# Kernel tuning notes

Measured on AMD Instinct MI355X. Metric: run time of the kernel, lower is better.

## Reference

```python
import jax, jax.numpy as jnp
import numpy as np

DIM = 1024
HEADS = 16
DH = DIM // HEADS          # 64
SEQ_LEN = 4096
LATENT = 1024
HIST = SEQ_LEN - LATENT    # 3072
LN_EPS = 1e-5


def setup_inputs() -> dict:
    key = jax.random.key(0)
    ks = jax.random.split(key, 5)
    b = 2
    x = jax.random.normal(ks[0], (b, SEQ_LEN, DIM), dtype=jnp.float32)
    s = 0.02
    Wq = jax.random.normal(ks[1], (DIM, DIM), dtype=jnp.float32) * s
    Wkv = jax.random.normal(ks[2], (DIM, DIM), dtype=jnp.float32) * s
    Wo = jax.random.normal(ks[3], (DIM, DIM), dtype=jnp.float32) * s
    bo = jnp.zeros((DIM,), dtype=jnp.float32)
    gamma = jnp.ones((DH,), dtype=jnp.float32)
    beta = jnp.zeros((DH,), dtype=jnp.float32)
    return {"x": x, "Wq": Wq, "Wkv": Wkv, "Wo": Wo, "bo": bo,
            "gamma": gamma, "beta": beta}


def _rotate_half(t):
    t1, t2 = jnp.split(t, 2, axis=-1)
    return jnp.concatenate([-t2, t1], axis=-1)


def reference(x, Wq, Wkv, Wo, bo, gamma, beta):
    b, n, dim = x.shape
    # projections (nn.Linear: y = x @ W.T), split heads -> (b, h, n, d)
    q = jnp.einsum('bnd,ed->bne', x, Wq).reshape(b, n, HEADS, DH).transpose(0, 2, 1, 3)
    kv = jnp.einsum('bnd,ed->bne', x, Wkv).reshape(b, n, HEADS, DH).transpose(0, 2, 1, 3)

    # layer_num == 0: queries only for the latent segment
    q = q[:, :, HIST:, :]  # (b, h, latent, d)

    # rotary embeddings: concat-style freqs over head dim
    inv_freq = 1.0 / (10000.0 ** (jnp.arange(0, DH, 2, dtype=jnp.float32) / DH))
    freqs = jnp.arange(n, dtype=jnp.float32)[:, None] * inv_freq[None, :]  # (n, DH/2)
    emb = jnp.concatenate([freqs, freqs], axis=-1)  # (n, DH)
    cos, sin = jnp.cos(emb), jnp.sin(emb)
    q = q * cos[HIST:] + _rotate_half(q) * sin[HIST:]
    kv = kv * cos + _rotate_half(kv) * sin

    q = q * (DH ** -0.5)

    # per-kv LayerNorm over head dim
    mu = kv.mean(axis=-1, keepdims=True)
    var = ((kv - mu) ** 2).mean(axis=-1, keepdims=True)
    kvn = (kv - mu) * jax.lax.rsqrt(var + LN_EPS) * gamma + beta

    attn = jnp.einsum('bhid,bhjd->bhij', q, kvn)  # (b, h, latent, n)

    # causal mask only on latent columns: col j (>= HIST) masked if j-HIST > i
    i = jnp.arange(LATENT)[:, None]
    j = jnp.arange(n)[None, :]
    mask = (j - HIST) > i  # false for history columns (j < HIST)
    neg = -jnp.finfo(attn.dtype).max
    attn = jnp.where(mask, neg, attn)

    attn = jax.nn.softmax(attn, axis=-1)
    out = jnp.einsum('bhij,bhjd->bhid', attn, kvn)  # (b, h, latent, d)
    out = out.transpose(0, 2, 1, 3).reshape(b, LATENT, dim)
    return jnp.einsum('bnd,ed->bne', out, Wo) + bo
```

## Files before the change

kernel.cpp:

```cpp
#include <hip/hip_runtime.h>
#include <hip/hip_bf16.h>
#include <cstdint>

#define DIMC 1024
#define HEADS 16
#define DHH 64
#define SEQ 4096
#define LATENT 1024
#define HISTC 3072
#define BATCH 2

typedef __attribute__((ext_vector_type(8))) __bf16 bf16x8;
typedef __attribute__((ext_vector_type(4))) float f32x4;
typedef __attribute__((ext_vector_type(16))) float f32x16;

__global__ void k_prep(const float* __restrict__ x, const float* __restrict__ Wq,
                       const float* __restrict__ Wkv, const float* __restrict__ Wo,
                       __bf16* __restrict__ x16, __bf16* __restrict__ wq16,
                       __bf16* __restrict__ wkv16, __bf16* __restrict__ wo16,
                       float2* __restrict__ cs) {
  int bidx = blockIdx.x;
  if (bidx < 2048) {
    int base = bidx * 256 + threadIdx.x;
#pragma unroll
    for (int k = 0; k < 4; ++k) {
      int i = base + k * 524288;
      float4 v = reinterpret_cast<const float4*>(x)[i];
      union { __bf16 h[4]; uint64_t u; } p;
      p.h[0] = (__bf16)v.x; p.h[1] = (__bf16)v.y;
      p.h[2] = (__bf16)v.z; p.h[3] = (__bf16)v.w;
      reinterpret_cast<uint64_t*>(x16)[i] = p.u;
    }
  } else if (bidx < 3584) {
    int id = bidx - 2048;
    const float* src; __bf16* dst;
    if (id < 512) { src = Wq; dst = wq16; }
    else if (id < 1024) { src = Wkv; dst = wkv16; id -= 512; }
    else { src = Wo; dst = wo16; id -= 1024; }
#pragma unroll
    for (int k = 0; k < 2; ++k) {
      int idx = id * 512 + k * 256 + threadIdx.x;
      float4 v = reinterpret_cast<const float4*>(src)[idx];
      union { __bf16 h[4]; uint64_t u; } p;
      p.h[0] = (__bf16)v.x; p.h[1] = (__bf16)v.y;
      p.h[2] = (__bf16)v.z; p.h[3] = (__bf16)v.w;
      reinterpret_cast<uint64_t*>(dst)[idx] = p.u;
    }
  } else {
    int idx = (bidx - 3584) * 256 + threadIdx.x;
    int pos = idx >> 5, f = idx & 31;
    float invf = exp2f(-(float)f * 0.41524101186f);
    float s, c;
    sincosf((float)pos * invf, &s, &c);
    cs[idx] = make_float2(c, s);
  }
}

__device__ __forceinline__ void gload16(void* lds, const void* g) {
  __builtin_amdgcn_global_load_lds(
      (const __attribute__((address_space(1))) unsigned int*)g,
      (__attribute__((address_space(3))) unsigned int*)lds, 16, 0, 0);
}

template<int BIAS>
__launch_bounds__(256)
__global__ void k_gemm(const __bf16* __restrict__ A, const __bf16* __restrict__ Bw,
                       float* __restrict__ C, const float* __restrict__ bias,
                       int M, int N, int K) {
  __shared__ __align__(16) char lds[32768];
  const int t = threadIdx.x;
  const int l = t & 63, w = t >> 6;
  const int wr = w >> 1, wc = w & 1;
  const int mblocks = M >> 7;
  const int m0 = (blockIdx.x % mblocks) * 128, n0 = (blockIdx.x / mblocks) * 128;
  const int lrow = l & 15, lk = l >> 4;
  f32x4 acc[4][4] = {};

  for (int k0 = 0; k0 < K; k0 += 64) {
    if (k0) __syncthreads();
#pragma unroll
    for (int i = 0; i < 4; ++i) {
      int c = i * 256 + t;
      int row = c >> 3;
      int kgc = ((c & 7) ^ (row & 7)) * 8;
      gload16(lds + c * 16, A + (size_t)(m0 + row) * K + k0 + kgc);
      gload16(lds + 16384 + c * 16, Bw + (size_t)(n0 + row) * K + k0 + kgc);
    }
    __syncthreads();
#pragma unroll
    for (int ks = 0; ks < 2; ++ks) {
      bf16x8 af[4], bfr[4];
#pragma unroll
      for (int m = 0; m < 4; ++m) {
        int row = wr * 64 + m * 16 + lrow;
        af[m] = *reinterpret_cast<const bf16x8*>(
            lds + row * 128 + ((ks * 4 + lk) ^ (row & 7)) * 16);
      }
#pragma unroll
      for (int n = 0; n < 4; ++n) {
        int row = wc * 64 + n * 16 + lrow;
        bfr[n] = *reinterpret_cast<const bf16x8*>(
            lds + 16384 + row * 128 + ((ks * 4 + lk) ^ (row & 7)) * 16);
      }
#pragma unroll
      for (int m = 0; m < 4; ++m)
#pragma unroll
        for (int n = 0; n < 4; ++n)
          acc[m][n] = __builtin_amdgcn_mfma_f32_16x16x32_bf16(af[m], bfr[n], acc[m][n], 0, 0, 0);
    }
  }

#pragma unroll
  for (int m = 0; m < 4; ++m)
#pragma unroll
    for (int n = 0; n < 4; ++n)
#pragma unroll
      for (int r = 0; r < 4; ++r) {
        int row = m0 + wr * 64 + m * 16 + (l >> 4) * 4 + r;
        int col = n0 + wc * 64 + n * 16 + (l & 15);
        float v = acc[m][n][r];
        if (BIAS) v += bias[col];
        C[(size_t)row * N + col] = v;
      }
}

__launch_bounds__(256)
__global__ void k_gemmqkv(const __bf16* __restrict__ x16,
                          const __bf16* __restrict__ wkv16,
                          const __bf16* __restrict__ wq16,
                          __bf16* __restrict__ kvn, __bf16* __restrict__ kvnT,
                          __bf16* __restrict__ qb,
                          const float* __restrict__ gamma,
                          const float* __restrict__ beta,
                          const float2* __restrict__ cstab) {
  __shared__ __align__(16) char lds[32768];
  const int t = threadIdx.x, l = t & 63, w = t >> 6;
  const int wr = w >> 1, wc = w & 1;
  const int by = blockIdx.x % 80;
  const bool isq = by >= 64;
  const int m0 = (isq ? (by - 64) : by) * 128;
  const int n0 = (blockIdx.x / 80) * 128;
  const __bf16* Bw = isq ? wq16 : wkv16;
  const int lrow = l & 15, lk = l >> 4;
  f32x4 acc[4][4] = {};

  for (int k0 = 0; k0 < 1024; k0 += 64) {
    if (k0) __syncthreads();
#pragma unroll
    for (int i = 0; i < 4; ++i) {
      int c = i * 256 + t;
      int row = c >> 3;
      int kgc = ((c & 7) ^ (row & 7)) * 8;
      int mi = m0 + row;
      if (isq) mi += HISTC + (mi >> 10) * HISTC;
      gload16(lds + c * 16, x16 + (size_t)mi * 1024 + k0 + kgc);
      gload16(lds + 16384 + c * 16, Bw + (size_t)(n0 + row) * 1024 + k0 + kgc);
    }
    __syncthreads();
#pragma unroll
    for (int ks = 0; ks < 2; ++ks) {
      bf16x8 af[4], bfr[4];
#pragma unroll
      for (int m = 0; m < 4; ++m) {
        int row = wr * 64 + m * 16 + lrow;
        af[m] = *reinterpret_cast<const bf16x8*>(
            lds + row * 128 + ((ks * 4 + lk) ^ (row & 7)) * 16);
      }
#pragma unroll
      for (int n = 0; n < 4; ++n) {
        int row = wc * 64 + n * 16 + lrow;
        bfr[n] = *reinterpret_cast<const bf16x8*>(
            lds + 16384 + row * 128 + ((ks * 4 + lk) ^ (row & 7)) * 16);
      }
#pragma unroll
      for (int m = 0; m < 4; ++m)
#pragma unroll
        for (int n = 0; n < 4; ++n)
          acc[m][n] = __builtin_amdgcn_mfma_f32_16x16x32_bf16(af[m], bfr[n], acc[m][n], 0, 0, 0);
    }
  }

#pragma unroll
  for (int m = 0; m < 4; ++m)
#pragma unroll
    for (int r = 0; r < 4; ++r) {
      int rl = wr * 64 + m * 16 + lk * 4 + r;
      int pos = isq ? (HISTC + ((m0 + rl) & 1023)) : ((m0 + rl) & 4095);
      float2 cs0 = cstab[pos * 32 + lrow];
      float2 cs1 = cstab[pos * 32 + 16 + lrow];
      float a0 = acc[m][0][r], a2 = acc[m][2][r];
      acc[m][0][r] = a0 * cs0.x - a2 * cs0.y;
      acc[m][2][r] = a2 * cs0.x + a0 * cs0.y;
      float a1 = acc[m][1][r], a3 = acc[m][3][r];
      acc[m][1][r] = a1 * cs1.x - a3 * cs1.y;
      acc[m][3][r] = a3 * cs1.x + a1 * cs1.y;
    }

  const int h = (n0 + wc * 64) >> 6;
  if (!isq) {
    float g4[4], b4[4];
#pragma unroll
    for (int n = 0; n < 4; ++n) { g4[n] = gamma[n * 16 + lrow]; b4[n] = beta[n * 16 + lrow]; }
#pragma unroll
    for (int m = 0; m < 4; ++m)
#pragma unroll
      for (int r = 0; r < 4; ++r) {
        float s1 = acc[m][0][r] + acc[m][1][r] + acc[m][2][r] + acc[m][3][r];
        float s2 = acc[m][0][r] * acc[m][0][r] + acc[m][1][r] * acc[m][1][r] +
                   acc[m][2][r] * acc[m][2][r] + acc[m][3][r] * acc[m][3][r];
#pragma unroll
        for (int mk = 1; mk < 16; mk <<= 1) {
          s1 += __shfl_xor(s1, mk);
          s2 += __shfl_xor(s2, mk);
        }
        float mu = s1 * 0.015625f;
        float var = s2 * 0.015625f - mu * mu;
        float inv = rsqrtf(var + 1e-5f);
#pragma unroll
        for (int n = 0; n < 4; ++n)
          acc[m][n][r] = (acc[m][n][r] - mu) * inv * g4[n] + b4[n];
      }
    const size_t hb = (size_t)((m0 >> 12) * HEADS + h);
#pragma unroll
    for (int m = 0; m < 4; ++m)
#pragma unroll
      for (int r = 0; r < 4; ++r) {
        int pos = (m0 + wr * 64 + m * 16 + lk * 4 + r) & 4095;
#pragma unroll
        for (int n = 0; n < 4; ++n)
          kvn[(hb * SEQ + pos) * DHH + n * 16 + lrow] = (__bf16)acc[m][n][r];
      }
#pragma unroll
    for (int m = 0; m < 4; ++m) {
      int pos0 = (m0 + wr * 64 + m * 16 + lk * 4) & 4095;
      int sp = (pos0 & ~12) | ((pos0 & 4) << 1) | ((pos0 & 8) >> 1);
#pragma unroll
      for (int n = 0; n < 4; ++n) {
        union { __bf16 hh[4]; uint64_t u; } pk;
#pragma unroll
        for (int r = 0; r < 4; ++r) pk.hh[r] = (__bf16)acc[m][n][r];
        *reinterpret_cast<uint64_t*>(kvnT + (hb * DHH + n * 16 + lrow) * SEQ + sp) = pk.u;
      }
    }
  } else {
    const size_t hb = (size_t)((m0 >> 10) * HEADS + h);
#pragma unroll
    for (int m = 0; m < 4; ++m)
#pragma unroll
      for (int r = 0; r < 4; ++r) {
        int qi = (m0 + wr * 64 + m * 16 + lk * 4 + r) & 1023;
#pragma unroll
        for (int n = 0; n < 4; ++n)
          qb[(hb * LATENT + qi) * DHH + n * 16 + lrow] =
              (__bf16)(acc[m][n][r] * 0.18033688011112042f);
      }
  }
}

__device__ __forceinline__ float fexp2(float x) {
#if __has_builtin(__builtin_amdgcn_exp2f)
  return __builtin_amdgcn_exp2f(x);
#else
  return exp2f(x);
#endif
}

__device__ __forceinline__ unsigned pk2(float a, float b) {
  union { __bf16 h[2]; unsigned u; } x;
  x.h[0] = (__bf16)a; x.h[1] = (__bf16)b;
  return x.u;
}

template<int NJ>
__launch_bounds__(256)
__global__ void k_flash12(const __bf16* __restrict__ qb, const __bf16* __restrict__ kvn,
                          const __bf16* __restrict__ kvnT, float* __restrict__ part) {
  const int bid = blockIdx.x;
  const int xcd = bid & 7;
  const int u = bid >> 3;
  const int jq = u % NJ;
  const int rest = u / NJ;
  int itq = rest & 7;
  const int grpb = rest >> 3;
  if (grpb >= 2) itq = 7 - itq;
  const int bh = xcd + 8 * grpb;
  const int h = bh & 15, b = bh >> 4;
  const int t = threadIdx.x, l = t & 63, w = t >> 6;
  const int q = l & 31, hi = l >> 5;
  const int iw0 = itq * 128;
  const int iwv = iw0 + w * 32;
  const int i = iwv + q;
  const __bf16* qbase = qb + ((size_t)(b * HEADS + h) * LATENT + iwv) * DHH;
  const __bf16* kbase = kvn + (size_t)(b * HEADS + h) * SEQ * DHH;
  const __bf16* vbase = kvnT + (size_t)(b * HEADS + h) * DHH * SEQ;

  __shared__ __align__(16) __bf16 Kl[2][2][32][64];
  __shared__ __align__(16) __bf16 Vl[2][2][64][32];

  const int krow = t >> 3, kgc = ((t & 7) ^ (krow & 7)) * 8;
  const int vrow = t >> 2, vgc = ((t & 3) ^ (vrow & 3)) * 8;

  bf16x8 qf[4];
#pragma unroll
  for (int c = 0; c < 4; ++c)
    qf[c] = *reinterpret_cast<const bf16x8*>(qbase + (size_t)q * DHH + c * 16 + hi * 8);

  const f32x16 Z = {};
  f32x16 O0 = {}, O1 = {};
  float m_run = -INFINITY, lacc = 0.f;

  const int ng = 2 * itq + 50;
  const int g0 = (ng * jq) / NJ, g1 = (ng * (jq + 1)) / NJ;
  const int sx = q & 3;

  {
    const int ja = g0 * 64;
    gload16((char*)&Kl[0][0][0][0] + t * 16, kbase + (size_t)(ja + krow) * DHH + kgc);
    gload16((char*)&Kl[0][1][0][0] + t * 16, kbase + (size_t)(ja + 32 + krow) * DHH + kgc);
    gload16((char*)&Vl[0][0][0][0] + t * 16, vbase + (size_t)vrow * SEQ + ja + vgc);
    gload16((char*)&Vl[0][1][0][0] + t * 16, vbase + (size_t)vrow * SEQ + ja + 32 + vgc);
  }
  __syncthreads();

  for (int g = g0; g < g1; ++g) {
    const int cur = (g - g0) & 1;
    const int ja = g * 64, jb = ja + 32;
    const char* Ka = (const char*)&Kl[cur][0][0][0];
    const char* Va = (const char*)&Vl[cur][0][0][0];
    bf16x8 kf0 = *reinterpret_cast<const bf16x8*>(Ka + q * 128 + ((0 + hi) ^ (q & 7)) * 16);
    bf16x8 kf1 = *reinterpret_cast<const bf16x8*>(Ka + q * 128 + ((2 + hi) ^ (q & 7)) * 16);
    bf16x8 kf2 = *reinterpret_cast<const bf16x8*>(Ka + q * 128 + ((4 + hi) ^ (q & 7)) * 16);
    bf16x8 kf3 = *reinterpret_cast<const bf16x8*>(Ka + q * 128 + ((6 + hi) ^ (q & 7)) * 16);
    f32x16 S = __builtin_amdgcn_mfma_f32_32x32x16_bf16(kf0, qf[0], Z, 0, 0, 0);
    S = __builtin_amdgcn_mfma_f32_32x32x16_bf16(kf1, qf[1], S, 0, 0, 0);
    S = __builtin_amdgcn_mfma_f32_32x32x16_bf16(kf2, qf[2], S, 0, 0, 0);
    S = __builtin_amdgcn_mfma_f32_32x32x16_bf16(kf3, qf[3], S, 0, 0, 0);
    if (g + 1 < g1) {
      const int jn = (g + 1) * 64;
      gload16((char*)&Kl[cur ^ 1][0][0][0] + t * 16, kbase + (size_t)(jn + krow) * DHH + kgc);
      gload16((char*)&Kl[cur ^ 1][1][0][0] + t * 16, kbase + (size_t)(jn + 32 + krow) * DHH + kgc);
      gload16((char*)&Vl[cur ^ 1][0][0][0] + t * 16, vbase + (size_t)vrow * SEQ + jn + vgc);
      gload16((char*)&Vl[cur ^ 1][1][0][0] + t * 16, vbase + (size_t)vrow * SEQ + jn + 32 + vgc);
    }
    if (ja + 31 > iwv + HISTC) {
#pragma unroll
      for (int r = 0; r < 16; ++r) {
        int j = ja + (r & 3) + 8 * (r >> 2) + 4 * hi;
        if (j > i + HISTC) S[r] = -1e30f;
      }
    }
    {
      float u1 = fmaxf(fmaxf(S[0], S[1]), S[2]);
      float u2 = fmaxf(fmaxf(S[3], S[4]), S[5]);
      float u3 = fmaxf(fmaxf(S[6], S[7]), S[8]);
      float u4 = fmaxf(fmaxf(S[9], S[10]), S[11]);
      float u5 = fmaxf(fmaxf(S[12], S[13]), S[14]);
      float pm = fmaxf(fmaxf(fmaxf(u1, u2), u3), fmaxf(fmaxf(u4, u5), S[15]));
      if (__any(pm > m_run + 8.0f)) {
        pm = fmaxf(pm, __shfl_xor(pm, 32));
        float mn = fmaxf(m_run, pm);
        float sc = fexp2(m_run - mn);
        m_run = mn;
        lacc *= sc;
#pragma unroll
        for (int r = 0; r < 16; ++r) { O0[r] *= sc; O1[r] *= sc; }
      }
      float p[16];
#pragma unroll
      for (int r = 0; r < 16; ++r) p[r] = fexp2(S[r] - m_run);
      float s8[8];
#pragma unroll
      for (int r = 0; r < 8; ++r) s8[r] = p[r] + p[r + 8];
      lacc += ((s8[0] + s8[4]) + (s8[1] + s8[5])) + ((s8[2] + s8[6]) + (s8[3] + s8[7]));
      union { unsigned u[4]; bf16x8 v; } pf0, pf1;
      pf0.u[0] = pk2(p[0], p[1]);   pf0.u[1] = pk2(p[2], p[3]);
      pf0.u[2] = pk2(p[4], p[5]);   pf0.u[3] = pk2(p[6], p[7]);
      pf1.u[0] = pk2(p[8], p[9]);   pf1.u[1] = pk2(p[10], p[11]);
      pf1.u[2] = pk2(p[12], p[13]); pf1.u[3] = pk2(p[14], p[15]);
      bf16x8 va00 = *reinterpret_cast<const bf16x8*>(Va + q * 64 + (hi ^ sx) * 16);
      bf16x8 va01 = *reinterpret_cast<const bf16x8*>(Va + q * 64 + ((2 + hi) ^ sx) * 16);
      bf16x8 va10 = *reinterpret_cast<const bf16x8*>(Va + (32 + q) * 64 + (hi ^ sx) * 16);
      bf16x8 va11 = *reinterpret_cast<const bf16x8*>(Va + (32 + q) * 64 + ((2 + hi) ^ sx) * 16);
      O0 = __builtin_amdgcn_mfma_f32_32x32x16_bf16(va00, pf0.v, O0, 0, 0, 0);
      O0 = __builtin_amdgcn_mfma_f32_32x32x16_bf16(va01, pf1.v, O0, 0, 0, 0);
      O1 = __builtin_amdgcn_mfma_f32_32x32x16_bf16(va10, pf0.v, O1, 0, 0, 0);
      O1 = __builtin_amdgcn_mfma_f32_32x32x16_bf16(va11, pf1.v, O1, 0, 0, 0);
    }
    const char* Kb = (const char*)&Kl[cur][1][0][0];
    const char* Vb = (const char*)&Vl[cur][1][0][0];
    bf16x8 kg0 = *reinterpret_cast<const bf16x8*>(Kb + q * 128 + ((0 + hi) ^ (q & 7)) * 16);
    bf16x8 kg1 = *reinterpret_cast<const bf16x8*>(Kb + q * 128 + ((2 + hi) ^ (q & 7)) * 16);
    bf16x8 kg2 = *reinterpret_cast<const bf16x8*>(Kb + q * 128 + ((4 + hi) ^ (q & 7)) * 16);
    bf16x8 kg3 = *reinterpret_cast<const bf16x8*>(Kb + q * 128 + ((6 + hi) ^ (q & 7)) * 16);
    f32x16 T = __builtin_amdgcn_mfma_f32_32x32x16_bf16(kg0, qf[0], Z, 0, 0, 0);
    T = __builtin_amdgcn_mfma_f32_32x32x16_bf16(kg1, qf[1], T, 0, 0, 0);
    T = __builtin_amdgcn_mfma_f32_32x32x16_bf16(kg2, qf[2], T, 0, 0, 0);
    T = __builtin_amdgcn_mfma_f32_32x32x16_bf16(kg3, qf[3], T, 0, 0, 0);
    if (jb + 31 > iwv + HISTC) {
#pragma unroll
      for (int r = 0; r < 16; ++r) {
        int j = jb + (r & 3) + 8 * (r >> 2) + 4 * hi;
        if (j > i + HISTC) T[r] = -1e30f;
      }
    }
    {
      float u1 = fmaxf(fmaxf(T[0], T[1]), T[2]);
      float u2 = fmaxf(fmaxf(T[3], T[4]), T[5]);
      float u3 = fmaxf(fmaxf(T[6], T[7]), T[8]);
      float u4 = fmaxf(fmaxf(T[9], T[10]), T[11]);
      float u5 = fmaxf(fmaxf(T[12], T[13]), T[14]);
      float pm = fmaxf(fmaxf(fmaxf(u1, u2), u3), fmaxf(fmaxf(u4, u5), T[15]));
      if (__any(pm > m_run + 8.0f)) {
        pm = fmaxf(pm, __shfl_xor(pm, 32));
        float mn = fmaxf(m_run, pm);
        float sc = fexp2(m_run - mn);
        m_run = mn;
        lacc *= sc;
#pragma unroll
        for (int r = 0; r < 16; ++r) { O0[r] *= sc; O1[r] *= sc; }
      }
      float p[16];
#pragma unroll
      for (int r = 0; r < 16; ++r) p[r] = fexp2(T[r] - m_run);
      float s8[8];
#pragma unroll
      for (int r = 0; r < 8; ++r) s8[r] = p[r] + p[r + 8];
      lacc += ((s8[0] + s8[4]) + (s8[1] + s8[5])) + ((s8[2] + s8[6]) + (s8[3] + s8[7]));
      union { unsigned u[4]; bf16x8 v; } pf0, pf1;
      pf0.u[0] = pk2(p[0], p[1]);   pf0.u[1] = pk2(p[2], p[3]);
      pf0.u[2] = pk2(p[4], p[5]);   pf0.u[3] = pk2(p[6], p[7]);
      pf1.u[0] = pk2(p[8], p[9]);   pf1.u[1] = pk2(p[10], p[11]);
      pf1.u[2] = pk2(p[12], p[13]); pf1.u[3] = pk2(p[14], p[15]);
      bf16x8 vb00 = *reinterpret_cast<const bf16x8*>(Vb + q * 64 + (hi ^ sx) * 16);
      bf16x8 vb01 = *reinterpret_cast<const bf16x8*>(Vb + q * 64 + ((2 + hi) ^ sx) * 16);
      bf16x8 vb10 = *reinterpret_cast<const bf16x8*>(Vb + (32 + q) * 64 + (hi ^ sx) * 16);
      bf16x8 vb11 = *reinterpret_cast<const bf16x8*>(Vb + (32 + q) * 64 + ((2 + hi) ^ sx) * 16);
      O0 = __builtin_amdgcn_mfma_f32_32x32x16_bf16(vb00, pf0.v, O0, 0, 0, 0);
      O0 = __builtin_amdgcn_mfma_f32_32x32x16_bf16(vb01, pf1.v, O0, 0, 0, 0);
      O1 = __builtin_amdgcn_mfma_f32_32x32x16_bf16(vb10, pf0.v, O1, 0, 0, 0);
      O1 = __builtin_amdgcn_mfma_f32_32x32x16_bf16(vb11, pf1.v, O1, 0, 0, 0);
    }
    __syncthreads();
  }
  float l_run = lacc + __shfl_xor(lacc, 32);

  const int pidx = (bh * 8 + itq) * NJ + jq;
  float* pw = part + (size_t)(pidx * 4 + w) * 34 * 64;
#pragma unroll
  for (int r = 0; r < 16; ++r) pw[r * 64 + l] = O0[r];
#pragma unroll
  for (int r = 0; r < 16; ++r) pw[(16 + r) * 64 + l] = O1[r];
  pw[32 * 64 + l] = m_run;
  pw[33 * 64 + l] = l_run;
}

template<int NJ>
__global__ void k_fmerge12(const float* __restrict__ part, __bf16* __restrict__ aout) {
  const int u = blockIdx.x;
  const int bh = u >> 3, itq = u & 7;
  const int b = bh >> 4, h = bh & 15;
  const int t = threadIdx.x;
  const int w = t >> 6, sub = t & 63, q = sub & 31, hi = sub >> 5;
  const float* pp[NJ];
#pragma unroll
  for (int j = 0; j < NJ; ++j)
    pp[j] = part + (size_t)((u * NJ + j) * 4 + w) * 34 * 64;
  float mm = -INFINITY;
#pragma unroll
  for (int j = 0; j < NJ; ++j) mm = fmaxf(mm, pp[j][32 * 64 + sub]);
  float sc[NJ];
  float ll = 0.f;
#pragma unroll
  for (int j = 0; j < NJ; ++j) {
    sc[j] = fexp2(pp[j][32 * 64 + sub] - mm);
    ll += pp[j][33 * 64 + sub] * sc[j];
  }
  float inv = 1.f / ll;
  const int row = itq * 128 + w * 32 + q;
  __bf16* orow = aout + ((size_t)(b * LATENT) + row) * DIMC + h * DHH;
#pragma unroll
  for (int g = 0; g < 4; ++g) {
    union { __bf16 hh[4]; uint2 u2; } pk;
#pragma unroll
    for (int e = 0; e < 4; ++e) {
      float o = 0.f;
#pragma unroll
      for (int j = 0; j < NJ; ++j) o += pp[j][(4 * g + e) * 64 + sub] * sc[j];
      pk.hh[e] = (__bf16)(o * inv);
    }
    *reinterpret_cast<uint2*>(orow + 8 * g + 4 * hi) = pk.u2;
#pragma unroll
    for (int e = 0; e < 4; ++e) {
      float o = 0.f;
#pragma unroll
      for (int j = 0; j < NJ; ++j) o += pp[j][(16 + 4 * g + e) * 64 + sub] * sc[j];
      pk.hh[e] = (__bf16)(o * inv);
    }
    *reinterpret_cast<uint2*>(orow + 32 + 8 * g + 4 * hi) = pk.u2;
  }
}

extern "C" void kernel_launch(void* const* d_in, const int* in_sizes, int n_in,
                              void* d_out, int out_size, void* d_ws, size_t ws_size,
                              hipStream_t stream) {
  const float* x = (const float*)d_in[0];
  const float* Wq = (const float*)d_in[1];
  const float* Wkv = (const float*)d_in[2];
  const float* Wo = (const float*)d_in[3];
  const float* bo = (const float*)d_in[4];
  const float* gamma = (const float*)d_in[5];
  const float* beta = (const float*)d_in[6];

  char* ws = (char*)d_ws;
  size_t o = 0;
  __bf16* x16 = (__bf16*)(ws + o);  o += (size_t)BATCH * SEQ * DIMC * 2;
  __bf16* wq16 = (__bf16*)(ws + o); o += (size_t)DIMC * DIMC * 2;
  __bf16* wkv16 = (__bf16*)(ws + o); o += (size_t)DIMC * DIMC * 2;
  __bf16* wo16 = (__bf16*)(ws + o); o += (size_t)DIMC * DIMC * 2;
  float2* cstab = (float2*)(ws + o); o += (size_t)SEQ * 32 * 8;
  __bf16* kvn = (__bf16*)(ws + o);  o += (size_t)BATCH * HEADS * SEQ * DHH * 2;
  __bf16* kvnT = (__bf16*)(ws + o); o += (size_t)BATCH * HEADS * SEQ * DHH * 2;
  __bf16* qb = (__bf16*)(ws + o);   o += (size_t)BATCH * HEADS * LATENT * DHH * 2;
  __bf16* aout = (__bf16*)(ws + o); o += (size_t)BATCH * LATENT * DIMC * 2;
  float* part = (float*)(ws + o);   o += (size_t)512 * 4 * 34 * 64 * 4;

  k_prep<<<4096, 256, 0, stream>>>(x, Wq, Wkv, Wo, x16, wq16, wkv16, wo16, cstab);
  k_gemmqkv<<<640, 256, 0, stream>>>(x16, wkv16, wq16, kvn, kvnT, qb, gamma, beta, cstab);
  k_flash12<2><<<512, 256, 0, stream>>>(qb, kvn, kvnT, part);
  k_fmerge12<2><<<256, 256, 0, stream>>>(part, aout);
  k_gemm<1><<<128, 256, 0, stream>>>(aout, wo16, (float*)d_out, bo, 2048, 1024, 1024);
}
```

Measured before the change: 141.3 us.

## Fuse split-KV merge into output projection GEMM and transpose partials via LDS

```diff
diff --git a/kernel.cpp b/kernel.cpp
--- a/kernel.cpp
+++ b/kernel.cpp
@@ -10,9 +10,26 @@
 #define HISTC 3072
 #define BATCH 2
 
+#define PSTR 68
+#define PBLK (128 * PSTR)
+
 typedef __attribute__((ext_vector_type(8))) __bf16 bf16x8;
 typedef __attribute__((ext_vector_type(4))) float f32x4;
 typedef __attribute__((ext_vector_type(16))) float f32x16;
+
+__device__ __forceinline__ float fexp2(float x) {
+#if __has_builtin(__builtin_amdgcn_exp2f)
+  return __builtin_amdgcn_exp2f(x);
+#else
+  return exp2f(x);
+#endif
+}
+
+__device__ __forceinline__ unsigned pk2(float a, float b) {
+  union { __bf16 h[2]; unsigned u; } x;
+  x.h[0] = (__bf16)a; x.h[1] = (__bf16)b;
+  return x.u;
+}
 
 __global__ void k_prep(const float* __restrict__ x, const float* __restrict__ Wq,
                        const float* __restrict__ Wkv, const float* __restrict__ Wo,
@@ -62,29 +79,50 @@
       (__attribute__((address_space(3))) unsigned int*)lds, 16, 0, 0);
 }
 
-template<int BIAS>
 __launch_bounds__(256)
-__global__ void k_gemm(const __bf16* __restrict__ A, const __bf16* __restrict__ Bw,
-                       float* __restrict__ C, const float* __restrict__ bias,
-                       int M, int N, int K) {
+__global__ void k_gemmo(const float* __restrict__ part, const __bf16* __restrict__ Bw,
+                        float* __restrict__ C, const float* __restrict__ bias) {
   __shared__ __align__(16) char lds[32768];
   const int t = threadIdx.x;
   const int l = t & 63, w = t >> 6;
   const int wr = w >> 1, wc = w & 1;
-  const int mblocks = M >> 7;
-  const int m0 = (blockIdx.x % mblocks) * 128, n0 = (blockIdx.x / mblocks) * 128;
+  const int mb = blockIdx.x & 15;
+  const int m0 = mb * 128, n0 = (blockIdx.x >> 4) * 128;
+  const int bb = mb >> 3, itq = mb & 7;
   const int lrow = l & 15, lk = l >> 4;
   f32x4 acc[4][4] = {};
 
-  for (int k0 = 0; k0 < K; k0 += 64) {
+  for (int k0 = 0; k0 < 1024; k0 += 64) {
     if (k0) __syncthreads();
+    const int h = k0 >> 6;
+    const float* pu = part + (size_t)(((bb * 16 + h) * 8 + itq) * 2) * PBLK;
 #pragma unroll
     for (int i = 0; i < 4; ++i) {
       int c = i * 256 + t;
       int row = c >> 3;
       int kgc = ((c & 7) ^ (row & 7)) * 8;
-      gload16(lds + c * 16, A + (size_t)(m0 + row) * K + k0 + kgc);
-      gload16(lds + 16384 + c * 16, Bw + (size_t)(n0 + row) * K + k0 + kgc);
+      const float* pr = pu + (size_t)row * PSTR;
+      float4 a0 = *reinterpret_cast<const float4*>(pr + kgc);
+      float4 a1 = *reinterpret_cast<const float4*>(pr + kgc + 4);
+      float4 b0 = *reinterpret_cast<const float4*>(pr + PBLK + kgc);
+      float4 b1 = *reinterpret_cast<const float4*>(pr + PBLK + kgc + 4);
+      float mA = pr[64], lA = pr[65];
+      float mB = pr[PBLK + 64], lB = pr[PBLK + 65];
+      float mm = fmaxf(mA, mB);
+      float sA = fexp2(mA - mm), sB = fexp2(mB - mm);
+      float inv = 1.f / (lA * sA + lB * sB);
+      sA *= inv; sB *= inv;
+      union { __bf16 hh[8]; uint4 u4; } pk;
+      pk.hh[0] = (__bf16)(a0.x * sA + b0.x * sB);
+      pk.hh[1] = (__bf16)(a0.y * sA + b0.y * sB);
+      pk.hh[2] = (__bf16)(a0.z * sA + b0.z * sB);
+      pk.hh[3] = (__bf16)(a0.w * sA + b0.w * sB);
+      pk.hh[4] = (__bf16)(a1.x * sA + b1.x * sB);
+      pk.hh[5] = (__bf16)(a1.y * sA + b1.y * sB);
+      pk.hh[6] = (__bf16)(a1.z * sA + b1.z * sB);
+      pk.hh[7] = (__bf16)(a1.w * sA + b1.w * sB);
+      *reinterpret_cast<uint4*>(lds + c * 16) = pk.u4;
+      gload16(lds + 16384 + c * 16, Bw + (size_t)(n0 + row) * 1024 + k0 + kgc);
     }
     __syncthreads();
 #pragma unroll
@@ -118,9 +156,7 @@
       for (int r = 0; r < 4; ++r) {
         int row = m0 + wr * 64 + m * 16 + (l >> 4) * 4 + r;
         int col = n0 + wc * 64 + n * 16 + (l & 15);
-        float v = acc[m][n][r];
-        if (BIAS) v += bias[col];
-        C[(size_t)row * N + col] = v;
+        C[(size_t)row * 1024 + col] = acc[m][n][r] + bias[col];
       }
 }
 
@@ -257,29 +293,14 @@
   }
 }
 
-__device__ __forceinline__ float fexp2(float x) {
-#if __has_builtin(__builtin_amdgcn_exp2f)
-  return __builtin_amdgcn_exp2f(x);
-#else
-  return exp2f(x);
-#endif
-}
-
-__device__ __forceinline__ unsigned pk2(float a, float b) {
-  union { __bf16 h[2]; unsigned u; } x;
-  x.h[0] = (__bf16)a; x.h[1] = (__bf16)b;
-  return x.u;
-}
-
-template<int NJ>
 __launch_bounds__(256)
-__global__ void k_flash12(const __bf16* __restrict__ qb, const __bf16* __restrict__ kvn,
+__global__ void k_flash13(const __bf16* __restrict__ qb, const __bf16* __restrict__ kvn,
                           const __bf16* __restrict__ kvnT, float* __restrict__ part) {
   const int bid = blockIdx.x;
   const int xcd = bid & 7;
   const int u = bid >> 3;
-  const int jq = u % NJ;
-  const int rest = u / NJ;
+  const int jq = u & 1;
+  const int rest = u >> 1;
   int itq = rest & 7;
   const int grpb = rest >> 3;
   if (grpb >= 2) itq = 7 - itq;
@@ -294,8 +315,11 @@
   const __bf16* kbase = kvn + (size_t)(b * HEADS + h) * SEQ * DHH;
   const __bf16* vbase = kvnT + (size_t)(b * HEADS + h) * DHH * SEQ;
 
-  __shared__ __align__(16) __bf16 Kl[2][2][32][64];
-  __shared__ __align__(16) __bf16 Vl[2][2][64][32];
+  __shared__ __align__(16) char smem[34816];
+  __shared__ float Mw[4][32];
+  __shared__ float Lw[4][32];
+  char* KlB = smem;
+  char* VlB = smem + 16384;
 
   const int krow = t >> 3, kgc = ((t & 7) ^ (krow & 7)) * 8;
   const int vrow = t >> 2, vgc = ((t & 3) ^ (vrow & 3)) * 8;
@@ -310,23 +334,23 @@
   float m_run = -INFINITY, lacc = 0.f;
 
   const int ng = 2 * itq + 50;
-  const int g0 = (ng * jq) / NJ, g1 = (ng * (jq + 1)) / NJ;
+  const int g0 = (ng * jq) >> 1, g1 = (ng * (jq + 1)) >> 1;
   const int sx = q & 3;
 
   {
     const int ja = g0 * 64;
-    gload16((char*)&Kl[0][0][0][0] + t * 16, kbase + (size_t)(ja + krow) * DHH + kgc);
-    gload16((char*)&Kl[0][1][0][0] + t * 16, kbase + (size_t)(ja + 32 + krow) * DHH + kgc);
-    gload16((char*)&Vl[0][0][0][0] + t * 16, vbase + (size_t)vrow * SEQ + ja + vgc);
-    gload16((char*)&Vl[0][1][0][0] + t * 16, vbase + (size_t)vrow * SEQ + ja + 32 + vgc);
+    gload16(KlB + t * 16, kbase + (size_t)(ja + krow) * DHH + kgc);
+    gload16(KlB + 4096 + t * 16, kbase + (size_t)(ja + 32 + krow) * DHH + kgc);
+    gload16(VlB + t * 16, vbase + (size_t)vrow * SEQ + ja + vgc);
+    gload16(VlB + 4096 + t * 16, vbase + (size_t)vrow * SEQ + ja + 32 + vgc);
   }
   __syncthreads();
 
   for (int g = g0; g < g1; ++g) {
     const int cur = (g - g0) & 1;
     const int ja = g * 64, jb = ja + 32;
-    const char* Ka = (const char*)&Kl[cur][0][0][0];
-    const char* Va = (const char*)&Vl[cur][0][0][0];
+    const char* Ka = KlB + cur * 8192;
+    const char* Va = VlB + cur * 8192;
     bf16x8 kf0 = *reinterpret_cast<const bf16x8*>(Ka + q * 128 + ((0 + hi) ^ (q & 7)) * 16);
     bf16x8 kf1 = *reinterpret_cast<const bf16x8*>(Ka + q * 128 + ((2 + hi) ^ (q & 7)) * 16);
     bf16x8 kf2 = *reinterpret_cast<const bf16x8*>(Ka + q * 128 + ((4 + hi) ^ (q & 7)) * 16);
@@ -337,10 +361,12 @@
     S = __builtin_amdgcn_mfma_f32_32x32x16_bf16(kf3, qf[3], S, 0, 0, 0);
     if (g + 1 < g1) {
       const int jn = (g + 1) * 64;
-      gload16((char*)&Kl[cur ^ 1][0][0][0] + t * 16, kbase + (size_t)(jn + krow) * DHH + kgc);
-      gload16((char*)&Kl[cur ^ 1][1][0][0] + t * 16, kbase + (size_t)(jn + 32 + krow) * DHH + kgc);
-      gload16((char*)&Vl[cur ^ 1][0][0][0] + t * 16, vbase + (size_t)vrow * SEQ + jn + vgc);
-      gload16((char*)&Vl[cur ^ 1][1][0][0] + t * 16, vbase + (size_t)vrow * SEQ + jn + 32 + vgc);
+      char* Kn = KlB + (cur ^ 1) * 8192;
+      char* Vn = VlB + (cur ^ 1) * 8192;
+      gload16(Kn + t * 16, kbase + (size_t)(jn + krow) * DHH + kgc);
+      gload16(Kn + 4096 + t * 16, kbase + (size_t)(jn + 32 + krow) * DHH + kgc);
+      gload16(Vn + t * 16, vbase + (size_t)vrow * SEQ + jn + vgc);
+      gload16(Vn + 4096 + t * 16, vbase + (size_t)vrow * SEQ + jn + 32 + vgc);
     }
     if (ja + 31 > iwv + HISTC) {
 #pragma unroll
@@ -386,8 +412,8 @@
       O1 = __builtin_amdgcn_mfma_f32_32x32x16_bf16(va10, pf0.v, O1, 0, 0, 0);
       O1 = __builtin_amdgcn_mfma_f32_32x32x16_bf16(va11, pf1.v, O1, 0, 0, 0);
     }
-    const char* Kb = (const char*)&Kl[cur][1][0][0];
-    const char* Vb = (const char*)&Vl[cur][1][0][0];
+    const char* Kb = KlB + cur * 8192 + 4096;
+    const char* Vb = VlB + cur * 8192 + 4096;
     bf16x8 kg0 = *reinterpret_cast<const bf16x8*>(Kb + q * 128 + ((0 + hi) ^ (q & 7)) * 16);
     bf16x8 kg1 = *reinterpret_cast<const bf16x8*>(Kb + q * 128 + ((2 + hi) ^ (q & 7)) * 16);
     bf16x8 kg2 = *reinterpret_cast<const bf16x8*>(Kb + q * 128 + ((4 + hi) ^ (q & 7)) * 16);
@@ -444,60 +470,23 @@
   }
   float l_run = lacc + __shfl_xor(lacc, 32);
 
-  const int pidx = (bh * 8 + itq) * NJ + jq;
-  float* pw = part + (size_t)(pidx * 4 + w) * 34 * 64;
-#pragma unroll
-  for (int r = 0; r < 16; ++r) pw[r * 64 + l] = O0[r];
-#pragma unroll
-  for (int r = 0; r < 16; ++r) pw[(16 + r) * 64 + l] = O1[r];
-  pw[32 * 64 + l] = m_run;
-  pw[33 * 64 + l] = l_run;
-}
-
-template<int NJ>
-__global__ void k_fmerge12(const float* __restrict__ part, __bf16* __restrict__ aout) {
-  const int u = blockIdx.x;
-  const int bh = u >> 3, itq = u & 7;
-  const int b = bh >> 4, h = bh & 15;
-  const int t = threadIdx.x;
-  const int w = t >> 6, sub = t & 63, q = sub & 31, hi = sub >> 5;
-  const float* pp[NJ];
-#pragma unroll
-  for (int j = 0; j < NJ; ++j)
-    pp[j] = part + (size_t)((u * NJ + j) * 4 + w) * 34 * 64;
-  float mm = -INFINITY;
-#pragma unroll
-  for (int j = 0; j < NJ; ++j) mm = fmaxf(mm, pp[j][32 * 64 + sub]);
-  float sc[NJ];
-  float ll = 0.f;
-#pragma unroll
-  for (int j = 0; j < NJ; ++j) {
-    sc[j] = fexp2(pp[j][32 * 64 + sub] - mm);
-    ll += pp[j][33 * 64 + sub] * sc[j];
-  }
-  float inv = 1.f / ll;
-  const int row = itq * 128 + w * 32 + q;
-  __bf16* orow = aout + ((size_t)(b * LATENT) + row) * DIMC + h * DHH;
-#pragma unroll
-  for (int g = 0; g < 4; ++g) {
-    union { __bf16 hh[4]; uint2 u2; } pk;
-#pragma unroll
-    for (int e = 0; e < 4; ++e) {
-      float o = 0.f;
-#pragma unroll
-      for (int j = 0; j < NJ; ++j) o += pp[j][(4 * g + e) * 64 + sub] * sc[j];
-      pk.hh[e] = (__bf16)(o * inv);
-    }
-    *reinterpret_cast<uint2*>(orow + 8 * g + 4 * hi) = pk.u2;
-#pragma unroll
-    for (int e = 0; e < 4; ++e) {
-      float o = 0.f;
-#pragma unroll
-      for (int j = 0; j < NJ; ++j) o += pp[j][(16 + 4 * g + e) * 64 + sub] * sc[j];
-      pk.hh[e] = (__bf16)(o * inv);
-    }
-    *reinterpret_cast<uint2*>(orow + 32 + 8 * g + 4 * hi) = pk.u2;
-  }
+  if (hi == 0) { Mw[w][q] = m_run; Lw[w][q] = l_run; }
+  float* Tw = reinterpret_cast<float*>(smem + (size_t)w * 8704);
+#pragma unroll
+  for (int r = 0; r < 16; ++r) {
+    int d = (r & 3) + 8 * (r >> 2) + 4 * hi;
+    Tw[q * PSTR + d] = O0[r];
+    Tw[q * PSTR + 32 + d] = O1[r];
+  }
+  __syncthreads();
+  const int pidx = (bh * 8 + itq) * 2 + jq;
+  const int row2 = l >> 1, half = l & 1;
+  float* dst = part + (size_t)pidx * PBLK + (size_t)(w * 32 + row2) * PSTR + half * 32;
+  const float* src = Tw + row2 * PSTR + half * 32;
+#pragma unroll
+  for (int e = 0; e < 8; ++e)
+    reinterpret_cast<float4*>(dst)[e] = reinterpret_cast<const float4*>(src)[e];
+  if (half == 0) { dst[64] = Mw[w][row2]; dst[65] = Lw[w][row2]; }
 }
 
 extern "C" void kernel_launch(void* const* d_in, const int* in_sizes, int n_in,
@@ -521,12 +510,10 @@
   __bf16* kvn = (__bf16*)(ws + o);  o += (size_t)BATCH * HEADS * SEQ * DHH * 2;
   __bf16* kvnT = (__bf16*)(ws + o); o += (size_t)BATCH * HEADS * SEQ * DHH * 2;
   __bf16* qb = (__bf16*)(ws + o);   o += (size_t)BATCH * HEADS * LATENT * DHH * 2;
-  __bf16* aout = (__bf16*)(ws + o); o += (size_t)BATCH * LATENT * DIMC * 2;
-  float* part = (float*)(ws + o);   o += (size_t)512 * 4 * 34 * 64 * 4;
+  float* part = (float*)(ws + o);   o += (size_t)512 * PBLK * 4;
 
   k_prep<<<4096, 256, 0, stream>>>(x, Wq, Wkv, Wo, x16, wq16, wkv16, wo16, cstab);
   k_gemmqkv<<<640, 256, 0, stream>>>(x16, wkv16, wq16, kvn, kvnT, qb, gamma, beta, cstab);
-  k_flash12<2><<<512, 256, 0, stream>>>(qb, kvn, kvnT, part);
-  k_fmerge12<2><<<256, 256, 0, stream>>>(part, aout);
-  k_gemm<1><<<128, 256, 0, stream>>>(aout, wo16, (float*)d_out, bo, 2048, 1024, 1024);
-}
+  k_flash13<<<512, 256, 0, stream>>>(qb, kvn, kvnT, part);
+  k_gemmo<<<128, 256, 0, stream>>>(part, wo16, (float*)d_out, bo);
+}
```

New measurement: 188.2 us. 33.1% more time.
